# Performance work log

Hardware: AMD Instinct MI355X
Metric: run time of the kernel (lower is better)

## Reference

```python
import jax, jax.numpy as jnp
import numpy as np

B, N, C = 8, 1025, 1024
H = 8
D = C // H  # 128
LORA = 16
TOK = 1024

def setup_inputs() -> dict:
    key = jax.random.key(0)
    ks = jax.random.split(key, 16)
    s = 0.02
    return {
        "x": jax.random.normal(ks[0], (B, N, C), jnp.float32),
        "style_k": jax.random.normal(ks[1], (B, N, C), jnp.float32),
        "style_v": jax.random.normal(ks[2], (B, N, C), jnp.float32),
        "W_qkv": jax.random.normal(ks[3], (C, 3 * C), jnp.float32) * s,
        "W_proj": jax.random.normal(ks[4], (C, C), jnp.float32) * s,
        "b_proj": jnp.zeros((C,), jnp.float32),
        "ak": jax.random.normal(ks[5], (TOK, LORA), jnp.float32) * s,
        "bk": jax.random.normal(ks[6], (LORA, C), jnp.float32) * s,
        "av": jax.random.normal(ks[7], (TOK, LORA), jnp.float32) * s,
        "bv": jax.random.normal(ks[8], (LORA, C), jnp.float32) * s,
        "W1": jax.random.normal(ks[9], (C, C // 4), jnp.float32) * s,
        "b1": jnp.zeros((C // 4,), jnp.float32),
        "W2": jax.random.normal(ks[10], (C // 4, 1), jnp.float32) * s,
        "b2": jnp.zeros((1,), jnp.float32),
    }

def reference(x, style_k, style_v, W_qkv, W_proj, b_proj, ak, bk, av, bv, W1, b1, W2, b2):
    Bx, Nx, Cx = x.shape
    # cls-token gating MLP over transposed patch tokens: cp has shape [B, C, N-1], N-1 == C
    cls_token = x[:, :1, :]                         # [B,1,C]
    cp = jnp.transpose(x[:, 1:, :], (0, 2, 1))      # [B,C,N-1]
    h = jax.nn.relu(cp @ W1 + b1)                   # [B,C,C//4]
    attn_w = jax.nn.sigmoid(h @ W2 + b2)            # [B,C,1]
    attn_w = attn_w[..., 0][:, None, :]             # [B,1,C]
    weighted_cls = cls_token * attn_w               # [B,1,C]

    qkv = (x @ W_qkv).reshape(Bx, Nx, 3, H, D)
    q, k, v = qkv[:, :, 0], qkv[:, :, 1], qkv[:, :, 2]  # each [B,N,H,D]

    tokens_k = ak @ bk                              # [TOK, C] (TOK == C)
    tokens_v = av @ bv
    lora_k = (style_k @ tokens_k.T).reshape(Bx, Nx, H, D)
    lora_v = (style_v @ tokens_v.T).reshape(Bx, Nx, H, D)

    kk = k + lora_k
    vv = v + lora_v
    scale = D ** -0.5  # xformers default softmax scale
    scores = jnp.einsum('bqhd,bkhd->bhqk', q, kk) * scale
    attn = jax.nn.softmax(scores, axis=-1)
    out = jnp.einsum('bhqk,bkhd->bqhd', attn, vv).reshape(Bx, Nx, Cx)
    out = out @ W_proj + b_proj

    x_return = jnp.concatenate([out[:, :1, :] + weighted_cls, out[:, 1:, :]], axis=1)
    return (x_return, vv)
```

## Files before the change

### kernel.cpp

```cpp
#include <hip/hip_runtime.h>
#include <hip/hip_bf16.h>
#include <stdint.h>

#define B_ 8
#define N_ 1025
#define C_ 1024
#define H_ 8
#define D_ 128
#define TOK_ 1024
#define LORA_ 16
#define M_ 8200
#define NPAD_ 1032

using bf16x8 = __attribute__((ext_vector_type(8))) short;
using f32x4  = __attribute__((ext_vector_type(4))) float;
typedef unsigned short u16;

__device__ __forceinline__ u16 f2bf(float f) {
    union { float f; unsigned u; } v; v.f = f;
    unsigned r = v.u + 0x7fffu + ((v.u >> 16) & 1u);
    return (u16)(r >> 16);
}

__device__ __forceinline__ unsigned cvt_pk_bf16(float lo, float hi) {
    unsigned r;
    asm("v_cvt_pk_bf16_f32 %0, %1, %2" : "=v"(r) : "v"(lo), "v"(hi));
    return r;
}

__device__ __forceinline__ void gload16(const u16* g, u16* l) {
    __builtin_amdgcn_global_load_lds(
        (const __attribute__((address_space(1))) void*)g,
        (__attribute__((address_space(3))) void*)l, 16, 0, 0);
}

__device__ __forceinline__ int xcd_swz(int bid, int nwg) {
    int cpx = nwg >> 3;
    return (bid & 7) * cpx + (bid >> 3);
}

__global__ __launch_bounds__(256) void cast3_kernel(
    const float* __restrict__ x, const float* __restrict__ sk, const float* __restrict__ sv,
    u16* __restrict__ xb, u16* __restrict__ skb, u16* __restrict__ svb)
{
    const float* in = blockIdx.y == 0 ? x : (blockIdx.y == 1 ? sk : sv);
    u16* out = blockIdx.y == 0 ? xb : (blockIdx.y == 1 ? skb : svb);
    size_t i = (size_t)blockIdx.x * 256 + threadIdx.x;
    float4 a = *((const float4*)in + i * 2);
    float4 b = *((const float4*)in + i * 2 + 1);
    bf16x8 v;
    v[0] = (short)f2bf(a.x); v[1] = (short)f2bf(a.y);
    v[2] = (short)f2bf(a.z); v[3] = (short)f2bf(a.w);
    v[4] = (short)f2bf(b.x); v[5] = (short)f2bf(b.y);
    v[6] = (short)f2bf(b.z); v[7] = (short)f2bf(b.w);
    *(bf16x8*)(out + i * 8) = v;
}

__global__ __launch_bounds__(256) void padcast16_kernel(
    const float* __restrict__ ak, const float* __restrict__ av,
    u16* __restrict__ akp, u16* __restrict__ avp)
{
    const float* in = blockIdx.y ? av : ak;
    u16* out = blockIdx.y ? avp : akp;
    int i = blockIdx.x * 256 + threadIdx.x;
    int t = i >> 4, l = i & 15;
    out[(size_t)t * 32 + l] = f2bf(in[i]);
    out[(size_t)t * 32 + 16 + l] = 0;
}

__global__ __launch_bounds__(256) void castb_kernel(
    const float* __restrict__ bk, const float* __restrict__ bv,
    u16* __restrict__ bkb, u16* __restrict__ bvb)
{
    const float* in = blockIdx.y ? bv : bk;
    u16* out = blockIdx.y ? bvb : bkb;
    int i = blockIdx.x * 256 + threadIdx.x;
    out[i] = f2bf(in[i]);
}

__global__ __launch_bounds__(256) void lora16_mfma(
    const u16* __restrict__ skb, const u16* __restrict__ svb,
    const u16* __restrict__ bkb, const u16* __restrict__ bvb,
    u16* __restrict__ sk16p, u16* __restrict__ sv16p)
{
    const u16* sb = blockIdx.y ? svb : skb;
    const u16* bb = blockIdx.y ? bvb : bkb;
    u16* op = blockIdx.y ? sv16p : sk16p;
    const int lane = threadIdx.x & 63, wid = threadIdx.x >> 6;
    const int base = blockIdx.x * 64 + wid * 16;
    int ma = base + (lane & 15); if (ma > M_ - 1) ma = M_ - 1;
    const int l = lane & 15;
    const u16* arow = sb + (size_t)ma * C_ + (lane >> 4) * 8;
    const u16* brow = bb + (size_t)l * C_ + (lane >> 4) * 8;
    f32x4 acc = {0.f, 0.f, 0.f, 0.f};
#pragma unroll
    for (int k0 = 0; k0 < C_; k0 += 32) {
        bf16x8 af = *(const bf16x8*)(arow + k0);
        bf16x8 bf = *(const bf16x8*)(brow + k0);
        acc = __builtin_amdgcn_mfma_f32_16x16x32_bf16(af, bf, acc, 0, 0, 0);
    }
#pragma unroll
    for (int r = 0; r < 4; ++r) {
        int m = base + (lane >> 4) * 4 + r; if (m > M_ - 1) m = M_ - 1;
        op[(size_t)m * 32 + l] = f2bf(acc[r]);
        op[(size_t)m * 32 + 16 + l] = 0;
    }
}

__global__ __launch_bounds__(256) void wt_kernel(
    const float* __restrict__ in, u16* __restrict__ out, int K, int Nw)
{
    __shared__ float t[32][33];
    int n0 = blockIdx.x * 32, k0 = blockIdx.y * 32;
    int tx = threadIdx.x & 31, ty = threadIdx.x >> 5;
#pragma unroll
    for (int yy = 0; yy < 32; yy += 8)
        t[ty + yy][tx] = in[(size_t)(k0 + ty + yy) * Nw + n0 + tx];
    __syncthreads();
#pragma unroll
    for (int yy = 0; yy < 32; yy += 8)
        out[(size_t)(n0 + ty + yy) * K + k0 + tx] = f2bf(t[tx][ty + yy]);
}

__global__ __launch_bounds__(256) void xt_kernel(
    const float* __restrict__ x, u16* __restrict__ xT)
{
    __shared__ float tb[32][33];
    int t0 = blockIdx.x * 32, c0 = blockIdx.y * 32, b = blockIdx.z;
    int tx = threadIdx.x & 31, ty = threadIdx.x >> 5;
#pragma unroll
    for (int yy = 0; yy < 32; yy += 8)
        tb[ty + yy][tx] = x[((size_t)b * N_ + 1 + t0 + ty + yy) * C_ + c0 + tx];
    __syncthreads();
#pragma unroll
    for (int yy = 0; yy < 32; yy += 8)
        xT[((size_t)b * 1024 + c0 + ty + yy) * 1024 + t0 + tx] = f2bf(tb[tx][ty + yy]);
}

__global__ __launch_bounds__(256) void vvt_kernel(
    const float* __restrict__ vv, u16* __restrict__ vvT)
{
    __shared__ float t[32][33];
    int n0 = blockIdx.x * 32, d0 = blockIdx.y * 32, bh = blockIdx.z;
    int b = bh >> 3, h = bh & 7;
    int tx = threadIdx.x & 31, ty = threadIdx.x >> 5;
#pragma unroll
    for (int yy = 0; yy < 32; yy += 8) {
        int n = n0 + ty + yy; if (n > 1024) n = 1024;
        t[ty + yy][tx] = vv[((size_t)(b * N_) + n) * C_ + h * D_ + d0 + tx];
    }
    __syncthreads();
#pragma unroll
    for (int yy = 0; yy < 32; yy += 8) {
        int n = n0 + tx;
        if (n < NPAD_)
            vvT[((size_t)bh * D_ + d0 + ty + yy) * NPAD_ + n] = f2bf(t[tx][ty + yy]);
    }
}

__device__ __forceinline__ void stage_tile(
    const u16* __restrict__ base, int row0, int maxrow,
    u16* lds, int k0, int lane, int wid)
{
#pragma unroll
    for (int j = 0; j < 4; ++j) {
        int i = wid * 4 + j;
        int p = i * 1024 + 16 * lane;
        int row = p >> 7, cb = p & 127;
        int cbs = cb ^ ((row & 7) << 4);
        int gr = row0 + row; if (gr > maxrow) gr = maxrow;
        gload16(base + (size_t)gr * 1024 + k0 + (cbs >> 1), lds + i * 512);
    }
}

__device__ __forceinline__ void gemm_pass(
    const u16* __restrict__ A, const u16* __restrict__ Bt, int row0, int nb0,
    u16* As, u16* Bs, f32x4 acc[4][4],
    const int lane, const int wid, const int wr, const int wc)
{
    for (int k0 = 0; k0 < 1024; k0 += 64) {
        __syncthreads();
        stage_tile(A,  row0, M_ - 1,    As, k0, lane, wid);
        stage_tile(Bt, nb0,  (1 << 30), Bs, k0, lane, wid);
        __syncthreads();
#pragma unroll
        for (int ks = 0; ks < 2; ++ks) {
            bf16x8 af[4], bfr[4];
#pragma unroll
            for (int mi = 0; mi < 4; ++mi) {
                int r = wr * 64 + mi * 16 + (lane & 15);
                int byte = (r * 128 + ks * 64 + (lane >> 4) * 16) ^ ((r & 7) << 4);
                af[mi] = *(const bf16x8*)((const char*)As + byte);
            }
#pragma unroll
            for (int ni = 0; ni < 4; ++ni) {
                int r = wc * 64 + ni * 16 + (lane & 15);
                int byte = (r * 128 + ks * 64 + (lane >> 4) * 16) ^ ((r & 7) << 4);
                bfr[ni] = *(const bf16x8*)((const char*)Bs + byte);
            }
#pragma unroll
            for (int mi = 0; mi < 4; ++mi)
#pragma unroll
                for (int ni = 0; ni < 4; ++ni)
                    acc[mi][ni] = __builtin_amdgcn_mfma_f32_16x16x32_bf16(
                        af[mi], bfr[ni], acc[mi][ni], 0, 0, 0);
        }
    }
}

__global__ __launch_bounds__(256) void se_gemm(
    const u16* __restrict__ xT, const u16* __restrict__ W1T,
    const float* __restrict__ b1, const float* __restrict__ W2,
    float* __restrict__ gred)
{
    __shared__ u16 As[8192], Bs[8192];
    __shared__ float red[128];
    const int tid = threadIdx.x, lane = tid & 63, wid = tid >> 6;
    const int wr = wid >> 1, wc = wid & 1;
    const int row0 = blockIdx.x * 128;
    const int pass = blockIdx.y;
    if (tid < 128) red[tid] = 0.f;
    const f32x4 FZ = {0.f, 0.f, 0.f, 0.f};

    f32x4 acc[4][4];
#pragma unroll
    for (int mi = 0; mi < 4; ++mi)
#pragma unroll
        for (int ni = 0; ni < 4; ++ni) acc[mi][ni] = FZ;
    gemm_pass(xT, W1T, row0, pass * 128, As, Bs, acc, lane, wid, wr, wc);
#pragma unroll
    for (int mi = 0; mi < 4; ++mi) {
#pragma unroll
        for (int r = 0; r < 4; ++r) {
            float v = 0.f;
#pragma unroll
            for (int ni = 0; ni < 4; ++ni) {
                int j = pass * 128 + wc * 64 + ni * 16 + (lane & 15);
                float h = acc[mi][ni][r] + b1[j];
                v += fmaxf(h, 0.f) * W2[j];
            }
#pragma unroll
            for (int off = 1; off < 16; off <<= 1) v += __shfl_xor(v, off);
            if ((lane & 15) == 0)
                atomicAdd(&red[wr * 64 + mi * 16 + (lane >> 4) * 4 + r], v);
        }
    }
    __syncthreads();
    if (tid < 128) atomicAdd(&gred[row0 + tid], red[tid]);
}

__global__ __launch_bounds__(256) void se_fin(
    const float* __restrict__ gred, const float* __restrict__ b2,
    const float* __restrict__ x, float* __restrict__ wcls)
{
    int row = blockIdx.x * 256 + threadIdx.x;
    int b = row >> 10, c = row & 1023;
    wcls[row] = x[(size_t)b * N_ * C_ + c] / (1.f + expf(-(gred[row] + b2[0])));
}

__global__ __launch_bounds__(256) void qkv_gemm(
    const u16* __restrict__ xb, const u16* __restrict__ WqkvT,
    const u16* __restrict__ sk16p, const u16* __restrict__ sv16p,
    const u16* __restrict__ akp, const u16* __restrict__ avp,
    u16* __restrict__ qb, u16* __restrict__ kkb, float* __restrict__ vvout)
{
    __shared__ u16 As[8192], Bs[8192];
    const int tid = threadIdx.x, lane = tid & 63, wid = tid >> 6;
    const int wr = wid >> 1, wc = wid & 1;
    const int swz = xcd_swz(blockIdx.x, 65 * 24);
    const int row0 = (swz / 24) * 128;
    const int ct = swz % 24, region = ct >> 3;
    const int creg = (ct & 7) * 128;
    const f32x4 FZ = {0.f, 0.f, 0.f, 0.f};
    f32x4 acc[4][4];
#pragma unroll
    for (int mi = 0; mi < 4; ++mi)
#pragma unroll
        for (int ni = 0; ni < 4; ++ni) acc[mi][ni] = FZ;

    gemm_pass(xb, WqkvT, row0, ct * 128, As, Bs, acc, lane, wid, wr, wc);

    if (region >= 1) {
        const u16* a16 = (region == 1) ? sk16p : sv16p;
        const u16* b16 = (region == 1) ? akp : avp;
        bf16x8 af2[4], bf2v[4];
#pragma unroll
        for (int mi = 0; mi < 4; ++mi) {
            int gr = row0 + wr * 64 + mi * 16 + (lane & 15);
            if (gr > M_ - 1) gr = M_ - 1;
            af2[mi] = *(const bf16x8*)(a16 + (size_t)gr * 32 + (lane >> 4) * 8);
        }
#pragma unroll
        for (int ni = 0; ni < 4; ++ni) {
            int gc = creg + wc * 64 + ni * 16 + (lane & 15);
            bf2v[ni] = *(const bf16x8*)(b16 + (size_t)gc * 32 + (lane >> 4) * 8);
        }
#pragma unroll
        for (int mi = 0; mi < 4; ++mi)
#pragma unroll
            for (int ni = 0; ni < 4; ++ni)
                acc[mi][ni] = __builtin_amdgcn_mfma_f32_16x16x32_bf16(
                    af2[mi], bf2v[ni], acc[mi][ni], 0, 0, 0);
    }

    const float QSCALE = 0.1275006182f;
#pragma unroll
    for (int mi = 0; mi < 4; ++mi) {
#pragma unroll
        for (int r = 0; r < 4; ++r) {
            int gr = row0 + wr * 64 + mi * 16 + (lane >> 4) * 4 + r;
            if (gr >= M_) continue;
#pragma unroll
            for (int ni = 0; ni < 4; ++ni) {
                int gc = creg + wc * 64 + ni * 16 + (lane & 15);
                float v = acc[mi][ni][r];
                if (region == 0)      qb [(size_t)gr * C_ + gc] = f2bf(v * QSCALE);
                else if (region == 1) kkb[(size_t)gr * C_ + gc] = f2bf(v);
                else                  vvout[(size_t)gr * C_ + gc] = v;
            }
        }
    }
}

__global__ __launch_bounds__(256) void proj_gemm(
    const u16* __restrict__ ob, const u16* __restrict__ WprojT,
    const float* __restrict__ bias, const float* __restrict__ wcls,
    float* __restrict__ outp)
{
    __shared__ u16 As[8192], Bs[8192];
    const int tid = threadIdx.x, lane = tid & 63, wid = tid >> 6;
    const int wr = wid >> 1, wc = wid & 1;
    const int swz = xcd_swz(blockIdx.x, 65 * 8);
    const int row0 = (swz / 8) * 128;
    const int ct = swz % 8;
    const f32x4 FZ = {0.f, 0.f, 0.f, 0.f};
    f32x4 acc[4][4];
#pragma unroll
    for (int mi = 0; mi < 4; ++mi)
#pragma unroll
        for (int ni = 0; ni < 4; ++ni) acc[mi][ni] = FZ;

    gemm_pass(ob, WprojT, row0, ct * 128, As, Bs, acc, lane, wid, wr, wc);

#pragma unroll
    for (int mi = 0; mi < 4; ++mi) {
#pragma unroll
        for (int r = 0; r < 4; ++r) {
            int gr = row0 + wr * 64 + mi * 16 + (lane >> 4) * 4 + r;
            if (gr >= M_) continue;
#pragma unroll
            for (int ni = 0; ni < 4; ++ni) {
                int gc = ct * 128 + wc * 64 + ni * 16 + (lane & 15);
                float v = acc[mi][ni][r] + bias[gc];
                if (gr % N_ == 0) v += wcls[(gr / N_) * C_ + gc];
                outp[(size_t)gr * C_ + gc] = v;
            }
        }
    }
}

__device__ __forceinline__ int psw(int pr, int colb) {
    return (pr * 128 + colb) ^ ((pr & 7) << 4) ^ ((pr & 8) << 2);
}

__global__ __launch_bounds__(256) void attn_kernel(
    const u16* __restrict__ qb, const u16* __restrict__ kkb,
    const u16* __restrict__ vvT, u16* __restrict__ ob)
{
    __shared__ u16 Ks[8192];
    __shared__ u16 Vs[8192];
    __shared__ u16 Ps[4096];
    const int tid = threadIdx.x, lane = tid & 63, wid = tid >> 6;
    const int swz = xcd_swz(blockIdx.x, 17 * 64);
    const int qt = swz % 17, bh = swz / 17, b = bh >> 3, h = bh & 7;
    const int n0q = qt * 64;
    const float THR = 11.54f;
    const u16* kbase = kkb + (size_t)b * N_ * C_ + h * D_;
    const u16* vbase = vvT + (size_t)bh * D_ * NPAD_;

    bf16x8 qf[4];
    {
        int qrow = n0q + wid * 16 + (lane & 15); if (qrow > 1024) qrow = 1024;
        const u16* qbase = qb + (size_t)(b * N_ + qrow) * C_ + h * D_ + (lane >> 4) * 8;
#pragma unroll
        for (int ks = 0; ks < 4; ++ks) qf[ks] = *(const bf16x8*)(qbase + ks * 32);
    }

    const int rowK = wid * 16 + (lane >> 4);
    const int cbsE = ((lane & 15) * 16) ^ ((rowK & 7) << 4);
    const u16* kpe = kbase + (size_t)rowK * C_ + (cbsE >> 1);
    const u16* kpo = kbase + (size_t)(rowK + 4) * C_ + ((cbsE ^ 64) >> 1);
    const int rowV = wid * 32 + (lane >> 3);
    const int cbsV = ((lane & 7) * 16) ^ ((rowV & 7) << 4);
    const u16* vp = vbase + (size_t)rowV * NPAD_ + (cbsV >> 1);

    const bf16x8 ones = {0x3F80, 0x3F80, 0x3F80, 0x3F80, 0x3F80, 0x3F80, 0x3F80, 0x3F80};
    float mrow[4];
    const f32x4 FZ = {0.f, 0.f, 0.f, 0.f};
    f32x4 of[8], lsacc = FZ;
#pragma unroll
    for (int r = 0; r < 4; ++r) mrow[r] = -3e38f;
#pragma unroll
    for (int ct = 0; ct < 8; ++ct) of[ct] = FZ;

    char* psb = (char*)Ps + wid * 2048;

    for (int t = 0; t < 17; ++t) {
        __syncthreads();
        gload16(kpe,              Ks + (wid * 4 + 0) * 512);
        gload16(kpo,              Ks + (wid * 4 + 1) * 512);
        gload16(kpe + 8 * C_,     Ks + (wid * 4 + 2) * 512);
        gload16(kpo + 8 * C_,     Ks + (wid * 4 + 3) * 512);
        gload16(vp,               Vs + (wid * 4 + 0) * 512);
        gload16(vp + 8 * NPAD_,   Vs + (wid * 4 + 1) * 512);
        gload16(vp + 16 * NPAD_,  Vs + (wid * 4 + 2) * 512);
        gload16(vp + 24 * NPAD_,  Vs + (wid * 4 + 3) * 512);
        kpe += 64 * C_; kpo += 64 * C_; vp += 64;
        __syncthreads();

        f32x4 s[4];
        __builtin_amdgcn_s_setprio(1);
#pragma unroll
        for (int jt = 0; jt < 4; ++jt) {
            f32x4 a = FZ;
#pragma unroll
            for (int ks = 0; ks < 4; ++ks) {
                int kvr = jt * 16 + (lane & 15);
                int byte = (kvr * 256 + ks * 64 + (lane >> 4) * 16) ^ ((kvr & 7) << 4);
                bf16x8 kf = *(const bf16x8*)((const char*)Ks + byte);
                a = __builtin_amdgcn_mfma_f32_16x16x32_bf16(qf[ks], kf, a, 0, 0, 0);
            }
            s[jt] = a;
        }
        __builtin_amdgcn_s_setprio(0);
        if (t == 16) {
#pragma unroll
            for (int jt = 0; jt < 4; ++jt) {
                int kvglob = 1024 + jt * 16 + (lane & 15);
                if (kvglob > 1024) {
                    s[jt][0] = -3e38f; s[jt][1] = -3e38f;
                    s[jt][2] = -3e38f; s[jt][3] = -3e38f;
                }
            }
        }

        float rmax[4];
#pragma unroll
        for (int r = 0; r < 4; ++r)
            rmax[r] = fmaxf(fmaxf(s[0][r], s[1][r]), fmaxf(s[2][r], s[3][r]));
        float g = fmaxf(fmaxf(rmax[0], rmax[1]), fmaxf(rmax[2], rmax[3]));
#pragma unroll
        for (int off = 1; off < 16; off <<= 1) g = fmaxf(g, __shfl_xor(g, off));
        int need = 0;
#pragma unroll
        for (int r = 0; r < 4; ++r) need |= (g > mrow[r] + THR) ? 1 : 0;

        if (__any(need)) {
            float al[4];
#pragma unroll
            for (int r = 0; r < 4; ++r) {
                float t0 = rmax[r];
#pragma unroll
                for (int off = 1; off < 16; off <<= 1) t0 = fmaxf(t0, __shfl_xor(t0, off));
                float mn = fmaxf(mrow[r], t0);
                al[r] = exp2f(mrow[r] - mn);
                mrow[r] = mn;
            }
#pragma unroll
            for (int ct = 0; ct < 8; ++ct)
#pragma unroll
                for (int r = 0; r < 4; ++r) of[ct][r] *= al[r];
#pragma unroll
            for (int r = 0; r < 4; ++r) lsacc[r] *= al[r];
        }
#pragma unroll
        for (int jt = 0; jt < 4; ++jt)
#pragma unroll
            for (int r = 0; r < 4; ++r) s[jt][r] = exp2f(s[jt][r] - mrow[r]);

#pragma unroll
        for (int jt = 0; jt < 4; ++jt) {
            unsigned pk01 = cvt_pk_bf16(s[jt][0], s[jt][1]);
            unsigned pk23 = cvt_pk_bf16(s[jt][2], s[jt][3]);
            int colb = (jt * 16 + (lane & 15)) * 2;
            int pr0 = (lane >> 4) * 4;
            *(u16*)(psb + psw(pr0,     colb)) = (u16)pk01;
            *(u16*)(psb + psw(pr0 + 1, colb)) = (u16)(pk01 >> 16);
            *(u16*)(psb + psw(pr0 + 2, colb)) = (u16)pk23;
            *(u16*)(psb + psw(pr0 + 3, colb)) = (u16)(pk23 >> 16);
        }

        bf16x8 pa[2];
#pragma unroll
        for (int ks2 = 0; ks2 < 2; ++ks2) {
            int prr = lane & 15;
            pa[ks2] = *(const bf16x8*)(psb + psw(prr, ks2 * 64 + (lane >> 4) * 16));
        }

        __builtin_amdgcn_s_setprio(1);
        lsacc = __builtin_amdgcn_mfma_f32_16x16x32_bf16(pa[0], ones, lsacc, 0, 0, 0);
        lsacc = __builtin_amdgcn_mfma_f32_16x16x32_bf16(pa[1], ones, lsacc, 0, 0, 0);
#pragma unroll
        for (int ct = 0; ct < 8; ++ct)
#pragma unroll
            for (int ks2 = 0; ks2 < 2; ++ks2) {
                int d = ct * 16 + (lane & 15);
                int byte = (d * 128 + ks2 * 64 + (lane >> 4) * 16) ^ ((d & 7) << 4);
                bf16x8 vf = *(const bf16x8*)((const char*)Vs + byte);
                of[ct] = __builtin_amdgcn_mfma_f32_16x16x32_bf16(pa[ks2], vf, of[ct], 0, 0, 0);
            }
        __builtin_amdgcn_s_setprio(0);
    }

#pragma unroll
    for (int ct = 0; ct < 8; ++ct)
#pragma unroll
        for (int r = 0; r < 4; ++r) {
            int n = n0q + wid * 16 + (lane >> 4) * 4 + r;
            if (n <= 1024)
                ob[(size_t)(b * N_ + n) * C_ + h * D_ + ct * 16 + (lane & 15)] =
                    f2bf(of[ct][r] / lsacc[r]);
        }
}

extern "C" void kernel_launch(void* const* d_in, const int* in_sizes, int n_in,
                              void* d_out, int out_size, void* d_ws, size_t ws_size,
                              hipStream_t stream)
{
    const float* x       = (const float*)d_in[0];
    const float* style_k = (const float*)d_in[1];
    const float* style_v = (const float*)d_in[2];
    const float* W_qkv   = (const float*)d_in[3];
    const float* W_proj  = (const float*)d_in[4];
    const float* b_proj  = (const float*)d_in[5];
    const float* ak      = (const float*)d_in[6];
    const float* bk      = (const float*)d_in[7];
    const float* av      = (const float*)d_in[8];
    const float* bv      = (const float*)d_in[9];
    const float* W1      = (const float*)d_in[10];
    const float* b1      = (const float*)d_in[11];
    const float* W2      = (const float*)d_in[12];
    const float* b2      = (const float*)d_in[13];

    float* outp   = (float*)d_out;
    float* vv_out = outp + (size_t)M_ * C_;

    u16* WqkvT = (u16*)outp;
    u16* xbb   = WqkvT + (size_t)3072 * 1024;
    u16* W1T   = xbb + (size_t)M_ * C_;
    u16* akp   = W1T + (size_t)256 * 1024;
    u16* avp   = akp + 1024 * 32;
    u16* bkb   = avp + 1024 * 32;
    u16* bvb   = bkb + 16 * 1024;
    u16* sk16p = bvb + 16 * 1024;
    u16* sv16p = sk16p + (size_t)M_ * 32;

    u16* ws     = (u16*)d_ws;
    u16* qb     = ws;
    u16* kkb    = qb  + (size_t)M_ * C_;
    u16* obuf   = kkb + (size_t)M_ * C_;
    u16* vvT    = obuf + (size_t)M_ * C_;
    u16* WprojT = vvT + (size_t)B_ * H_ * D_ * NPAD_;
    float* wcls = (float*)(WprojT + (size_t)1024 * 1024);
    float* gred = wcls + 8192;
    u16* skb = obuf;
    u16* svb = vvT;
    u16* xT  = qb;

    wt_kernel<<<dim3(96, 32), 256, 0, stream>>>(W_qkv, WqkvT, 1024, 3072);
    wt_kernel<<<dim3(32, 32), 256, 0, stream>>>(W_proj, WprojT, 1024, 1024);
    wt_kernel<<<dim3(8, 32), 256, 0, stream>>>(W1, W1T, 1024, 256);
    padcast16_kernel<<<dim3(64, 2), 256, 0, stream>>>(ak, av, akp, avp);
    castb_kernel<<<dim3(64, 2), 256, 0, stream>>>(bk, bv, bkb, bvb);
    cast3_kernel<<<dim3(4100, 3), 256, 0, stream>>>(x, style_k, style_v, xbb, skb, svb);
    xt_kernel<<<dim3(32, 32, 8), 256, 0, stream>>>(x, xT);
    hipMemsetAsync(gred, 0, 8192 * sizeof(float), stream);
    se_gemm<<<dim3(64, 2), 256, 0, stream>>>(xT, W1T, b1, W2, gred);
    se_fin<<<dim3(32), 256, 0, stream>>>(gred, b2, x, wcls);
    lora16_mfma<<<dim3(129, 2), 256, 0, stream>>>(skb, svb, bkb, bvb, sk16p, sv16p);

    qkv_gemm<<<dim3(65 * 24), 256, 0, stream>>>(xbb, WqkvT, sk16p, sv16p, akp, avp,
                                                qb, kkb, vv_out);
    vvt_kernel<<<dim3(33, 4, 64), 256, 0, stream>>>(vv_out, vvT);
    attn_kernel<<<dim3(17 * 64), 256, 0, stream>>>(qb, kkb, vvT, obuf);
    proj_gemm<<<dim3(65 * 8), 256, 0, stream>>>(obuf, WprojT, b_proj, wcls, outp);
}
```

Before: 342.6 us.

## Widen QKV and proj GEMM tiles to 128x256 with 512-thread blocks

The QKV and output-projection GEMMs now use 512-thread blocks, each computing a 128x256 output tile, which halves the number of workgroups and reuses each staged A tile across twice as many columns. A new staging routine spreads the loads over 8 waves, and a generalized XCD swizzle handles grid sizes not divisible by 8. The goal is less redundant A-tile global traffic per output. The cost is more LDS per block and fewer blocks, which may hurt occupancy or leave CUs idle at the wave tail (780 and 260 blocks).

```diff
diff --git a/kernel.cpp b/kernel.cpp
--- a/kernel.cpp
+++ b/kernel.cpp
@@ -37,6 +37,11 @@
 __device__ __forceinline__ int xcd_swz(int bid, int nwg) {
     int cpx = nwg >> 3;
     return (bid & 7) * cpx + (bid >> 3);
+}
+__device__ __forceinline__ int xcd_swz_g(int bid, int nwg) {
+    int q = nwg >> 3, r = nwg & 7;
+    int xcd = bid & 7, i = bid >> 3;
+    return (xcd < r ? xcd * (q + 1) : r * (q + 1) + (xcd - r) * q) + i;
 }
 
 __global__ __launch_bounds__(256) void cast3_kernel(
@@ -208,6 +213,57 @@
     }
 }
 
+template<int NSEG>
+__device__ __forceinline__ void stage_tile512(
+    const u16* __restrict__ base, int row0, int maxrow,
+    u16* lds, int k0, int lane, int wid)
+{
+#pragma unroll
+    for (int j = 0; j < NSEG; ++j) {
+        int i = wid * NSEG + j;
+        int p = i * 1024 + 16 * lane;
+        int row = p >> 7, cb = p & 127;
+        int cbs = cb ^ ((row & 7) << 4);
+        int gr = row0 + row; if (gr > maxrow) gr = maxrow;
+        gload16(base + (size_t)gr * 1024 + k0 + (cbs >> 1), lds + i * 512);
+    }
+}
+
+__device__ __forceinline__ void gemm_pass512(
+    const u16* __restrict__ A, const u16* __restrict__ Bt, int row0, int nb0,
+    u16* As, u16* Bs, f32x4 acc[4][4],
+    const int lane, const int wid, const int wr, const int wc)
+{
+    for (int k0 = 0; k0 < 1024; k0 += 64) {
+        __syncthreads();
+        stage_tile512<2>(A,  row0, M_ - 1,    As, k0, lane, wid);
+        stage_tile512<4>(Bt, nb0,  (1 << 30), Bs, k0, lane, wid);
+        __syncthreads();
+#pragma unroll
+        for (int ks = 0; ks < 2; ++ks) {
+            bf16x8 af[4], bfr[4];
+#pragma unroll
+            for (int mi = 0; mi < 4; ++mi) {
+                int r = wr * 64 + mi * 16 + (lane & 15);
+                int byte = (r * 128 + ks * 64 + (lane >> 4) * 16) ^ ((r & 7) << 4);
+                af[mi] = *(const bf16x8*)((const char*)As + byte);
+            }
+#pragma unroll
+            for (int ni = 0; ni < 4; ++ni) {
+                int r = wc * 64 + ni * 16 + (lane & 15);
+                int byte = (r * 128 + ks * 64 + (lane >> 4) * 16) ^ ((r & 7) << 4);
+                bfr[ni] = *(const bf16x8*)((const char*)Bs + byte);
+            }
+#pragma unroll
+            for (int mi = 0; mi < 4; ++mi)
+#pragma unroll
+                for (int ni = 0; ni < 4; ++ni)
+                    acc[mi][ni] = __builtin_amdgcn_mfma_f32_16x16x32_bf16(
+                        af[mi], bfr[ni], acc[mi][ni], 0, 0, 0);
+        }
+    }
+}
+
 __global__ __launch_bounds__(256) void se_gemm(
     const u16* __restrict__ xT, const u16* __restrict__ W1T,
     const float* __restrict__ b1, const float* __restrict__ W2,
@@ -258,19 +314,19 @@
     wcls[row] = x[(size_t)b * N_ * C_ + c] / (1.f + expf(-(gred[row] + b2[0])));
 }
 
-__global__ __launch_bounds__(256) void qkv_gemm(
+__global__ __launch_bounds__(512) void qkv_gemm(
     const u16* __restrict__ xb, const u16* __restrict__ WqkvT,
     const u16* __restrict__ sk16p, const u16* __restrict__ sv16p,
     const u16* __restrict__ akp, const u16* __restrict__ avp,
     u16* __restrict__ qb, u16* __restrict__ kkb, float* __restrict__ vvout)
 {
-    __shared__ u16 As[8192], Bs[8192];
+    __shared__ u16 As[8192], Bs[16384];
     const int tid = threadIdx.x, lane = tid & 63, wid = tid >> 6;
-    const int wr = wid >> 1, wc = wid & 1;
-    const int swz = xcd_swz(blockIdx.x, 65 * 24);
-    const int row0 = (swz / 24) * 128;
-    const int ct = swz % 24, region = ct >> 3;
-    const int creg = (ct & 7) * 128;
+    const int wr = wid >> 2, wc = wid & 3;
+    const int swz = xcd_swz_g(blockIdx.x, 65 * 12);
+    const int row0 = (swz / 12) * 128;
+    const int ct = swz % 12, region = ct >> 2;
+    const int creg = (ct & 3) * 256;
     const f32x4 FZ = {0.f, 0.f, 0.f, 0.f};
     f32x4 acc[4][4];
 #pragma unroll
@@ -278,7 +334,7 @@
 #pragma unroll
         for (int ni = 0; ni < 4; ++ni) acc[mi][ni] = FZ;
 
-    gemm_pass(xb, WqkvT, row0, ct * 128, As, Bs, acc, lane, wid, wr, wc);
+    gemm_pass512(xb, WqkvT, row0, region * 1024 + creg, As, Bs, acc, lane, wid, wr, wc);
 
     if (region >= 1) {
         const u16* a16 = (region == 1) ? sk16p : sv16p;
@@ -322,17 +378,17 @@
     }
 }
 
-__global__ __launch_bounds__(256) void proj_gemm(
+__global__ __launch_bounds__(512) void proj_gemm(
     const u16* __restrict__ ob, const u16* __restrict__ WprojT,
     const float* __restrict__ bias, const float* __restrict__ wcls,
     float* __restrict__ outp)
 {
-    __shared__ u16 As[8192], Bs[8192];
+    __shared__ u16 As[8192], Bs[16384];
     const int tid = threadIdx.x, lane = tid & 63, wid = tid >> 6;
-    const int wr = wid >> 1, wc = wid & 1;
-    const int swz = xcd_swz(blockIdx.x, 65 * 8);
-    const int row0 = (swz / 8) * 128;
-    const int ct = swz % 8;
+    const int wr = wid >> 2, wc = wid & 3;
+    const int swz = xcd_swz_g(blockIdx.x, 65 * 4);
+    const int row0 = (swz / 4) * 128;
+    const int ct = swz % 4;
     const f32x4 FZ = {0.f, 0.f, 0.f, 0.f};
     f32x4 acc[4][4];
 #pragma unroll
@@ -340,7 +396,7 @@
 #pragma unroll
         for (int ni = 0; ni < 4; ++ni) acc[mi][ni] = FZ;
 
-    gemm_pass(ob, WprojT, row0, ct * 128, As, Bs, acc, lane, wid, wr, wc);
+    gemm_pass512(ob, WprojT, row0, ct * 256, As, Bs, acc, lane, wid, wr, wc);
 
 #pragma unroll
     for (int mi = 0; mi < 4; ++mi) {
@@ -350,7 +406,7 @@
             if (gr >= M_) continue;
 #pragma unroll
             for (int ni = 0; ni < 4; ++ni) {
-                int gc = ct * 128 + wc * 64 + ni * 16 + (lane & 15);
+                int gc = ct * 256 + wc * 64 + ni * 16 + (lane & 15);
                 float v = acc[mi][ni][r] + bias[gc];
                 if (gr % N_ == 0) v += wcls[(gr / N_) * C_ + gc];
                 outp[(size_t)gr * C_ + gc] = v;
@@ -579,9 +635,9 @@
     se_fin<<<dim3(32), 256, 0, stream>>>(gred, b2, x, wcls);
     lora16_mfma<<<dim3(129, 2), 256, 0, stream>>>(skb, svb, bkb, bvb, sk16p, sv16p);
 
-    qkv_gemm<<<dim3(65 * 24), 256, 0, stream>>>(xbb, WqkvT, sk16p, sv16p, akp, avp,
+    qkv_gemm<<<dim3(65 * 12), 512, 0, stream>>>(xbb, WqkvT, sk16p, sv16p, akp, avp,
                                                 qb, kkb, vv_out);
     vvt_kernel<<<dim3(33, 4, 64), 256, 0, stream>>>(vv_out, vvT);
     attn_kernel<<<dim3(17 * 64), 256, 0, stream>>>(qb, kkb, vvT, obuf);
-    proj_gemm<<<dim3(65 * 8), 256, 0, stream>>>(obuf, WprojT, b_proj, wcls, outp);
-}
+    proj_gemm<<<dim3(65 * 4), 512, 0, stream>>>(obuf, WprojT, b_proj, wcls, outp);
+}
```

Measured after the change: 308.7 us. -9.9%, faster.
